# Kernel tuning notes

Hardware: AMD Instinct MI355X
Metric: run time of the kernel (lower is better)

The kernel has to match this reference:

```python
import jax, jax.numpy as jnp
import numpy as np

N_NODES = 40000
FEAT = 128
HID = 128
EMB = 64
N_EDGES = 640000


def setup_inputs() -> dict:
    key = jax.random.key(0)
    ks = jax.random.split(key, 8)
    x = jax.random.normal(ks[0], (N_NODES, FEAT), dtype=jnp.float32)
    edge_index = jax.random.randint(ks[1], (2, N_EDGES), 0, N_NODES, dtype=jnp.int64)
    s1 = 1.0 / np.sqrt(FEAT)
    s2 = 1.0 / np.sqrt(HID)
    W1_l = jax.random.uniform(ks[2], (HID, FEAT), jnp.float32, -s1, s1)
    b1 = jax.random.uniform(ks[3], (HID,), jnp.float32, -s1, s1)
    W1_r = jax.random.uniform(ks[4], (HID, FEAT), jnp.float32, -s1, s1)
    W2_l = jax.random.uniform(ks[5], (EMB, HID), jnp.float32, -s2, s2)
    b2 = jax.random.uniform(ks[6], (EMB,), jnp.float32, -s2, s2)
    W2_r = jax.random.uniform(ks[7], (EMB, HID), jnp.float32, -s2, s2)
    return {"x": x, "edge_index": edge_index, "W1_l": W1_l, "b1": b1,
            "W1_r": W1_r, "W2_l": W2_l, "b2": b2, "W2_r": W2_r}


def _sage_conv(x, src, dst, W_l, b_l, W_r, n_nodes):
    # mean aggregation of source-node features onto destination nodes
    msg = x[src]                                           # [E, d]
    agg = jax.ops.segment_sum(msg, dst, num_segments=n_nodes)   # [N, d]
    cnt = jax.ops.segment_sum(jnp.ones((src.shape[0],), x.dtype), dst,
                              num_segments=n_nodes)        # [N]
    agg = agg / jnp.maximum(cnt, 1.0)[:, None]
    # out = lin_l(mean_j x_j) + lin_r(x_i); bias lives in lin_l
    return agg @ W_l.T + b_l + x @ W_r.T


def reference(x, edge_index, W1_l, b1, W1_r, W2_l, b2, W2_r):
    src, dst = edge_index[0], edge_index[1]
    n = x.shape[0]
    h = _sage_conv(x, src, dst, W1_l, b1, W1_r, n)
    h = jax.nn.elu(h)
    # dropout p=0.2 is identity in eval mode
    h = _sage_conv(h, src, dst, W2_l, b2, W2_r, n)
    return jax.nn.log_softmax(h, axis=1)
```

## Files before the change

### kernel.cpp

```cpp
#include <hip/hip_runtime.h>
#include <hip/hip_fp16.h>
#include <math.h>

#define N_NODES 40000
#define FEATD 128
#define EMB 64
#define N_EDGES 640000
#define CAP 64
#define NB 79
#define NFB 625
#define SEGCAP 48

typedef unsigned short u16;
typedef unsigned char u8;
typedef unsigned int u32;
typedef __attribute__((ext_vector_type(8))) unsigned short u16x8;
typedef __attribute__((ext_vector_type(8))) _Float16 f16x8;
typedef __attribute__((ext_vector_type(4))) float f32x4;
typedef __attribute__((ext_vector_type(2))) float f32x2;
typedef __attribute__((ext_vector_type(2))) unsigned int u32x2;

__device__ __forceinline__ float h2f(u16 h) {
  __half hh;
  *(u16*)&hh = h;
  return __half2float(hh);
}
__device__ __forceinline__ u16 f2h(float f) {
  __half hh = __float2half(f);
  return *(u16*)&hh;
}

__global__ __launch_bounds__(256) void prep_fill_kernel(
    const float* __restrict__ x, const float* __restrict__ W1l,
    const float* __restrict__ W1r, const float* __restrict__ W2l,
    const float* __restrict__ W2r, const int* __restrict__ src,
    const int* __restrict__ dst, u16* __restrict__ xh, u8* __restrict__ xq,
    u16* __restrict__ wp, u32* __restrict__ est, u16* __restrict__ cnts) {
  __shared__ int hist[NB], starts[NB], scan[NB], cnt2[NB];
  __shared__ u32 staging[1024];
  int bid = blockIdx.x;
  int tid = threadIdx.x;
  if (bid < NFB) {
    if (tid < NB) { hist[tid] = 0; cnt2[tid] = 0; }
    __syncthreads();
    int t = bid * 256 + tid;
    int4 s4 = *(const int4*)(&src[t * 4]);
    int4 d4 = *(const int4*)(&dst[t * 4]);
    int b0 = d4.x >> 9, b1 = d4.y >> 9, b2 = d4.z >> 9, b3 = d4.w >> 9;
    atomicAdd(&hist[b0], 1); atomicAdd(&hist[b1], 1);
    atomicAdd(&hist[b2], 1); atomicAdd(&hist[b3], 1);
    __syncthreads();
    if (tid < NB) scan[tid] = hist[tid];
    for (int off = 1; off < NB; off <<= 1) {
      __syncthreads();
      int v = 0;
      if (tid < NB && tid >= off) v = scan[tid - off];
      __syncthreads();
      if (tid < NB) scan[tid] += v;
    }
    __syncthreads();
    if (tid < NB) starts[tid] = scan[tid] - hist[tid];
    __syncthreads();
    u32 e0 = ((u32)d4.x << 16) | (u32)s4.x;
    u32 e1 = ((u32)d4.y << 16) | (u32)s4.y;
    u32 e2 = ((u32)d4.z << 16) | (u32)s4.z;
    u32 e3 = ((u32)d4.w << 16) | (u32)s4.w;
    int p0 = starts[b0] + atomicAdd(&cnt2[b0], 1); staging[p0] = e0;
    int p1 = starts[b1] + atomicAdd(&cnt2[b1], 1); staging[p1] = e1;
    int p2 = starts[b2] + atomicAdd(&cnt2[b2], 1); staging[p2] = e2;
    int p3 = starts[b3] + atomicAdd(&cnt2[b3], 1); staging[p3] = e3;
    __syncthreads();
#pragma unroll
    for (int it = 0; it < 4; it++) {
      int i = tid + 256 * it;
      u32 e = staging[i];
      int b = (int)(e >> 25);
      int r = i - starts[b];
      if (r < SEGCAP) est[((size_t)b * NFB + bid) * SEGCAP + r] = e;
    }
    if (tid < NB) cnts[tid * NFB + bid] = (u16)hist[tid];
  } else if (bid < 3125) {
    int i = (bid - NFB) * 256 + tid;
    float4 v0 = *(const float4*)(&x[i * 8]);
    float4 v1 = *(const float4*)(&x[i * 8 + 4]);
    u16x8 o;
    o[0] = f2h(v0.x); o[1] = f2h(v0.y); o[2] = f2h(v0.z); o[3] = f2h(v0.w);
    o[4] = f2h(v1.x); o[5] = f2h(v1.y); o[6] = f2h(v1.z); o[7] = f2h(v1.w);
    *(u16x8*)(&xh[i * 8]) = o;
    u32 w0 = __builtin_amdgcn_cvt_pk_fp8_f32(v0.x, v0.y, 0u, false);
    w0 = __builtin_amdgcn_cvt_pk_fp8_f32(v0.z, v0.w, w0, true);
    u32 w1 = __builtin_amdgcn_cvt_pk_fp8_f32(v1.x, v1.y, 0u, false);
    w1 = __builtin_amdgcn_cvt_pk_fp8_f32(v1.z, v1.w, w1, true);
    u32x2 qo; qo.x = w0; qo.y = w1;
    *(u32x2*)(&xq[i * 8]) = qo;
  } else {
    int i = (bid - 3125) * 256 + tid;
    const float* srcp;
    int off;
    if (i < 16384)      { srcp = W1l; off = i; }
    else if (i < 32768) { srcp = W1r; off = i - 16384; }
    else if (i < 40960) { srcp = W2l; off = i - 32768; }
    else                { srcp = W2r; off = i - 40960; }
    wp[i] = f2h(srcp[off]);
  }
}

__global__ __launch_bounds__(512) void scatter_kernel(
    const u32* __restrict__ est, const u16* __restrict__ cnts,
    int* __restrict__ deg, u16* __restrict__ bucket) {
  __shared__ int ldeg[512];
  int b = blockIdx.x, tid = threadIdx.x;
  ldeg[tid] = 0;
  __syncthreads();
  int n0 = b << 9;
  for (int seg = tid; seg < NFB; seg += 512) {
    int c = cnts[b * NFB + seg];
    if (c > SEGCAP) c = SEGCAP;
    const u32* p = est + ((size_t)b * NFB + seg) * SEGCAP;
    for (int r = 0; r < c; r++) {
      u32 e = p[r];
      int l = (int)(e >> 16) - n0;
      int s = atomicAdd(&ldeg[l], 1);
      if (s < CAP) bucket[(size_t)(n0 + l) * CAP + s] = (u16)(e & 0xffff);
    }
  }
  __syncthreads();
  int n = n0 + tid;
  if (n < N_NODES) deg[n] = ldeg[tid];
}

__global__ __launch_bounds__(256) void gather_mean_f8(
    const u8* __restrict__ xq, const int* __restrict__ deg,
    const u16* __restrict__ bucket, u16* __restrict__ aggh) {
  int n = blockIdx.x * 4 + (threadIdx.x >> 6);
  int lane = threadIdx.x & 63;
  int g = lane >> 4;
  int li = lane & 15;
  int dgf = deg[n];
  int dg = dgf < CAP ? dgf : CAP;
  float inv = 1.0f / fmaxf((float)dgf, 1.0f);
  const u16* bk = bucket + n * CAP;
  float acc0[8], acc1[8], acc2[8], acc3[8];
#pragma unroll
  for (int i = 0; i < 8; i++) { acc0[i] = 0.f; acc1[i] = 0.f; acc2[i] = 0.f; acc3[i] = 0.f; }
  int d = g;
  for (; d + 12 < dg; d += 16) {
    u32x2 v0 = *(const u32x2*)(&xq[(size_t)bk[d] * 128 + li * 8]);
    u32x2 v1 = *(const u32x2*)(&xq[(size_t)bk[d + 4] * 128 + li * 8]);
    u32x2 v2 = *(const u32x2*)(&xq[(size_t)bk[d + 8] * 128 + li * 8]);
    u32x2 v3 = *(const u32x2*)(&xq[(size_t)bk[d + 12] * 128 + li * 8]);
    {
      f32x2 p0 = __builtin_amdgcn_cvt_pk_f32_fp8(v0.x, false);
      f32x2 p1 = __builtin_amdgcn_cvt_pk_f32_fp8(v0.x, true);
      f32x2 p2 = __builtin_amdgcn_cvt_pk_f32_fp8(v0.y, false);
      f32x2 p3 = __builtin_amdgcn_cvt_pk_f32_fp8(v0.y, true);
      acc0[0] += p0.x; acc0[1] += p0.y; acc0[2] += p1.x; acc0[3] += p1.y;
      acc0[4] += p2.x; acc0[5] += p2.y; acc0[6] += p3.x; acc0[7] += p3.y;
    }
    {
      f32x2 p0 = __builtin_amdgcn_cvt_pk_f32_fp8(v1.x, false);
      f32x2 p1 = __builtin_amdgcn_cvt_pk_f32_fp8(v1.x, true);
      f32x2 p2 = __builtin_amdgcn_cvt_pk_f32_fp8(v1.y, false);
      f32x2 p3 = __builtin_amdgcn_cvt_pk_f32_fp8(v1.y, true);
      acc1[0] += p0.x; acc1[1] += p0.y; acc1[2] += p1.x; acc1[3] += p1.y;
      acc1[4] += p2.x; acc1[5] += p2.y; acc1[6] += p3.x; acc1[7] += p3.y;
    }
    {
      f32x2 p0 = __builtin_amdgcn_cvt_pk_f32_fp8(v2.x, false);
      f32x2 p1 = __builtin_amdgcn_cvt_pk_f32_fp8(v2.x, true);
      f32x2 p2 = __builtin_amdgcn_cvt_pk_f32_fp8(v2.y, false);
      f32x2 p3 = __builtin_amdgcn_cvt_pk_f32_fp8(v2.y, true);
      acc2[0] += p0.x; acc2[1] += p0.y; acc2[2] += p1.x; acc2[3] += p1.y;
      acc2[4] += p2.x; acc2[5] += p2.y; acc2[6] += p3.x; acc2[7] += p3.y;
    }
    {
      f32x2 p0 = __builtin_amdgcn_cvt_pk_f32_fp8(v3.x, false);
      f32x2 p1 = __builtin_amdgcn_cvt_pk_f32_fp8(v3.x, true);
      f32x2 p2 = __builtin_amdgcn_cvt_pk_f32_fp8(v3.y, false);
      f32x2 p3 = __builtin_amdgcn_cvt_pk_f32_fp8(v3.y, true);
      acc3[0] += p0.x; acc3[1] += p0.y; acc3[2] += p1.x; acc3[3] += p1.y;
      acc3[4] += p2.x; acc3[5] += p2.y; acc3[6] += p3.x; acc3[7] += p3.y;
    }
  }
  for (; d + 4 < dg; d += 8) {
    u32x2 v0 = *(const u32x2*)(&xq[(size_t)bk[d] * 128 + li * 8]);
    u32x2 v1 = *(const u32x2*)(&xq[(size_t)bk[d + 4] * 128 + li * 8]);
    {
      f32x2 p0 = __builtin_amdgcn_cvt_pk_f32_fp8(v0.x, false);
      f32x2 p1 = __builtin_amdgcn_cvt_pk_f32_fp8(v0.x, true);
      f32x2 p2 = __builtin_amdgcn_cvt_pk_f32_fp8(v0.y, false);
      f32x2 p3 = __builtin_amdgcn_cvt_pk_f32_fp8(v0.y, true);
      acc0[0] += p0.x; acc0[1] += p0.y; acc0[2] += p1.x; acc0[3] += p1.y;
      acc0[4] += p2.x; acc0[5] += p2.y; acc0[6] += p3.x; acc0[7] += p3.y;
    }
    {
      f32x2 p0 = __builtin_amdgcn_cvt_pk_f32_fp8(v1.x, false);
      f32x2 p1 = __builtin_amdgcn_cvt_pk_f32_fp8(v1.x, true);
      f32x2 p2 = __builtin_amdgcn_cvt_pk_f32_fp8(v1.y, false);
      f32x2 p3 = __builtin_amdgcn_cvt_pk_f32_fp8(v1.y, true);
      acc1[0] += p0.x; acc1[1] += p0.y; acc1[2] += p1.x; acc1[3] += p1.y;
      acc1[4] += p2.x; acc1[5] += p2.y; acc1[6] += p3.x; acc1[7] += p3.y;
    }
  }
  if (d < dg) {
    u32x2 v0 = *(const u32x2*)(&xq[(size_t)bk[d] * 128 + li * 8]);
    f32x2 p0 = __builtin_amdgcn_cvt_pk_f32_fp8(v0.x, false);
    f32x2 p1 = __builtin_amdgcn_cvt_pk_f32_fp8(v0.x, true);
    f32x2 p2 = __builtin_amdgcn_cvt_pk_f32_fp8(v0.y, false);
    f32x2 p3 = __builtin_amdgcn_cvt_pk_f32_fp8(v0.y, true);
    acc0[0] += p0.x; acc0[1] += p0.y; acc0[2] += p1.x; acc0[3] += p1.y;
    acc0[4] += p2.x; acc0[5] += p2.y; acc0[6] += p3.x; acc0[7] += p3.y;
  }
#pragma unroll
  for (int i = 0; i < 8; i++) {
    acc0[i] += acc1[i] + acc2[i] + acc3[i];
    acc0[i] += __shfl_xor(acc0[i], 16);
    acc0[i] += __shfl_xor(acc0[i], 32);
  }
  if (g == 0) {
    u16x8 o;
#pragma unroll
    for (int i = 0; i < 8; i++) o[i] = f2h(acc0[i] * inv);
    *(u16x8*)(&aggh[n * 128 + li * 8]) = o;
  }
}

__global__ __launch_bounds__(256) void gemm12_kernel(
    const u16* __restrict__ AggH, const u16* __restrict__ XH,
    const u16* __restrict__ wp, const float* __restrict__ b1v,
    const float* __restrict__ b2v, u8* __restrict__ Yq,
    u16* __restrict__ Zh) {
  const u16* w1l = wp;
  const u16* w1r = wp + 16384;
  const u16* w2l = wp + 32768;
  const u16* w2r = wp + 40960;

  __shared__ __align__(16) union {
    struct {
      u16 wl[128][72], wr[128][72];
      u16 a[64][72], x[64][72];
    } p1;
    struct {
      u16 h[64][136];
      u16 w2l[64][136], w2r[64][136];
    } p2;
  } L;

  const int tid = threadIdx.x;
  const int wv = tid >> 6;
  const int lane = tid & 63;
  const int li = lane & 15;
  const int q = lane >> 4;
  const int nbase = blockIdx.x * 64;

  f32x4 acc1[8];
#pragma unroll
  for (int jt = 0; jt < 8; jt++) acc1[jt] = (f32x4){0.f, 0.f, 0.f, 0.f};

  for (int kb = 0; kb < 2; kb++) {
#pragma unroll
    for (int it = 0; it < 4; it++) {
      int idx = tid + 256 * it;
      int j = idx >> 3, c = idx & 7;
      int go = j * 128 + kb * 64 + c * 8;
      *(u16x8*)(&L.p1.wl[j][c * 8]) = *(const u16x8*)(&w1l[go]);
      *(u16x8*)(&L.p1.wr[j][c * 8]) = *(const u16x8*)(&w1r[go]);
    }
#pragma unroll
    for (int it = 0; it < 2; it++) {
      int idx = tid + 256 * it;
      int n = idx >> 3, c = idx & 7;
      int go = (nbase + n) * 128 + kb * 64 + c * 8;
      *(u16x8*)(&L.p1.a[n][c * 8]) = *(const u16x8*)(&AggH[go]);
      *(u16x8*)(&L.p1.x[n][c * 8]) = *(const u16x8*)(&XH[go]);
    }
    __syncthreads();
#pragma unroll
    for (int kk = 0; kk < 2; kk++) {
      f16x8 aF = *(const f16x8*)(&L.p1.a[wv * 16 + li][kk * 32 + q * 8]);
      f16x8 xF = *(const f16x8*)(&L.p1.x[wv * 16 + li][kk * 32 + q * 8]);
#pragma unroll
      for (int jt = 0; jt < 8; jt++) {
        f16x8 wlF = *(const f16x8*)(&L.p1.wl[jt * 16 + li][kk * 32 + q * 8]);
        f16x8 wrF = *(const f16x8*)(&L.p1.wr[jt * 16 + li][kk * 32 + q * 8]);
        acc1[jt] = __builtin_amdgcn_mfma_f32_16x16x32_f16(aF, wlF, acc1[jt], 0, 0, 0);
        acc1[jt] = __builtin_amdgcn_mfma_f32_16x16x32_f16(xF, wrF, acc1[jt], 0, 0, 0);
      }
    }
    __syncthreads();
  }

#pragma unroll
  for (int jt = 0; jt < 8; jt++) {
    int j = jt * 16 + li;
    float bb = b1v[j];
#pragma unroll
    for (int r = 0; r < 4; r++) {
      float v = acc1[jt][r] + bb;
      v = v > 0.f ? v : expm1f(v);
      L.p2.h[wv * 16 + q * 4 + r][j] = f2h(v);
    }
  }
#pragma unroll
  for (int it = 0; it < 4; it++) {
    int idx = tid + 256 * it;
    int j = idx >> 4, c = idx & 15;
    int go = j * 128 + c * 8;
    *(u16x8*)(&L.p2.w2l[j][c * 8]) = *(const u16x8*)(&w2l[go]);
    *(u16x8*)(&L.p2.w2r[j][c * 8]) = *(const u16x8*)(&w2r[go]);
  }
  __syncthreads();

  f32x4 accY[4], accZ[4];
#pragma unroll
  for (int mt = 0; mt < 4; mt++) {
    accY[mt] = (f32x4){0.f, 0.f, 0.f, 0.f};
    accZ[mt] = (f32x4){0.f, 0.f, 0.f, 0.f};
  }
#pragma unroll
  for (int kc = 0; kc < 4; kc++) {
    f16x8 blF = *(const f16x8*)(&L.p2.w2l[wv * 16 + li][kc * 32 + q * 8]);
    f16x8 brF = *(const f16x8*)(&L.p2.w2r[wv * 16 + li][kc * 32 + q * 8]);
#pragma unroll
    for (int mt = 0; mt < 4; mt++) {
      f16x8 hF = *(const f16x8*)(&L.p2.h[mt * 16 + li][kc * 32 + q * 8]);
      accY[mt] = __builtin_amdgcn_mfma_f32_16x16x32_f16(hF, blF, accY[mt], 0, 0, 0);
      accZ[mt] = __builtin_amdgcn_mfma_f32_16x16x32_f16(hF, brF, accZ[mt], 0, 0, 0);
    }
  }

  {
    int j2 = wv * 16 + li;
    float bb = b2v[j2];
#pragma unroll
    for (int mt = 0; mt < 4; mt++) {
#pragma unroll
      for (int r = 0; r < 4; r++) {
        int node = nbase + mt * 16 + q * 4 + r;
        float yv = accY[mt][r];
        u32 w = __builtin_amdgcn_cvt_pk_fp8_f32(yv, yv, 0u, false);
        Yq[node * 64 + j2] = (u8)w;
        Zh[node * 64 + j2] = f2h(accZ[mt][r] + bb);
      }
    }
  }
}

__global__ __launch_bounds__(256) void final_kernel(
    const u8* __restrict__ Yq, const u16* __restrict__ Zh,
    const int* __restrict__ deg, const u16* __restrict__ bucket,
    float* __restrict__ out) {
  int n = blockIdx.x * 4 + (threadIdx.x >> 6);
  int lane = threadIdx.x & 63;
  int g = lane >> 3;
  int li = lane & 7;
  int dgf = deg[n];
  int dg = dgf < CAP ? dgf : CAP;
  float inv = 1.0f / fmaxf((float)dgf, 1.0f);
  const u16* bk = bucket + n * CAP;
  float acc0[8], acc1[8];
#pragma unroll
  for (int i = 0; i < 8; i++) { acc0[i] = 0.f; acc1[i] = 0.f; }
  int d = g;
  for (; d + 8 < dg; d += 16) {
    u32x2 v0 = *(const u32x2*)(&Yq[(size_t)bk[d] * 64 + li * 8]);
    u32x2 v1 = *(const u32x2*)(&Yq[(size_t)bk[d + 8] * 64 + li * 8]);
    {
      f32x2 p0 = __builtin_amdgcn_cvt_pk_f32_fp8(v0.x, false);
      f32x2 p1 = __builtin_amdgcn_cvt_pk_f32_fp8(v0.x, true);
      f32x2 p2 = __builtin_amdgcn_cvt_pk_f32_fp8(v0.y, false);
      f32x2 p3 = __builtin_amdgcn_cvt_pk_f32_fp8(v0.y, true);
      acc0[0] += p0.x; acc0[1] += p0.y; acc0[2] += p1.x; acc0[3] += p1.y;
      acc0[4] += p2.x; acc0[5] += p2.y; acc0[6] += p3.x; acc0[7] += p3.y;
    }
    {
      f32x2 p0 = __builtin_amdgcn_cvt_pk_f32_fp8(v1.x, false);
      f32x2 p1 = __builtin_amdgcn_cvt_pk_f32_fp8(v1.x, true);
      f32x2 p2 = __builtin_amdgcn_cvt_pk_f32_fp8(v1.y, false);
      f32x2 p3 = __builtin_amdgcn_cvt_pk_f32_fp8(v1.y, true);
      acc1[0] += p0.x; acc1[1] += p0.y; acc1[2] += p1.x; acc1[3] += p1.y;
      acc1[4] += p2.x; acc1[5] += p2.y; acc1[6] += p3.x; acc1[7] += p3.y;
    }
  }
  if (d < dg) {
    u32x2 v0 = *(const u32x2*)(&Yq[(size_t)bk[d] * 64 + li * 8]);
    f32x2 p0 = __builtin_amdgcn_cvt_pk_f32_fp8(v0.x, false);
    f32x2 p1 = __builtin_amdgcn_cvt_pk_f32_fp8(v0.x, true);
    f32x2 p2 = __builtin_amdgcn_cvt_pk_f32_fp8(v0.y, false);
    f32x2 p3 = __builtin_amdgcn_cvt_pk_f32_fp8(v0.y, true);
    acc0[0] += p0.x; acc0[1] += p0.y; acc0[2] += p1.x; acc0[3] += p1.y;
    acc0[4] += p2.x; acc0[5] += p2.y; acc0[6] += p3.x; acc0[7] += p3.y;
  }
#pragma unroll
  for (int i = 0; i < 8; i++) {
    acc0[i] += acc1[i];
    acc0[i] += __shfl_xor(acc0[i], 8);
    acc0[i] += __shfl_xor(acc0[i], 16);
    acc0[i] += __shfl_xor(acc0[i], 32);
  }
  u16x8 zb = *(const u16x8*)(&Zh[n * 64 + li * 8]);
  float v[8];
#pragma unroll
  for (int i = 0; i < 8; i++) v[i] = h2f(zb[i]) + acc0[i] * inv;
  float m = v[0];
#pragma unroll
  for (int i = 1; i < 8; i++) m = fmaxf(m, v[i]);
  m = fmaxf(m, __shfl_xor(m, 1));
  m = fmaxf(m, __shfl_xor(m, 2));
  m = fmaxf(m, __shfl_xor(m, 4));
  float s = 0.f;
#pragma unroll
  for (int i = 0; i < 8; i++) s += __expf(v[i] - m);
  s += __shfl_xor(s, 1); s += __shfl_xor(s, 2); s += __shfl_xor(s, 4);
  float lg = m + logf(s);
  if (lane < 8) {
    float4 o0 = {v[0] - lg, v[1] - lg, v[2] - lg, v[3] - lg};
    float4 o1 = {v[4] - lg, v[5] - lg, v[6] - lg, v[7] - lg};
    *(float4*)(&out[n * 64 + li * 8]) = o0;
    *(float4*)(&out[n * 64 + li * 8 + 4]) = o1;
  }
}

extern "C" void kernel_launch(void* const* d_in, const int* in_sizes, int n_in,
                              void* d_out, int out_size, void* d_ws, size_t ws_size,
                              hipStream_t stream) {
  const float* x   = (const float*)d_in[0];
  const int*   ei  = (const int*)d_in[1];
  const float* W1l = (const float*)d_in[2];
  const float* b1  = (const float*)d_in[3];
  const float* W1r = (const float*)d_in[4];
  const float* W2l = (const float*)d_in[5];
  const float* b2  = (const float*)d_in[6];
  const float* W2r = (const float*)d_in[7];
  float* out = (float*)d_out;

  const int* src = ei;
  const int* dst = ei + N_EDGES;

  u16* bucket = (u16*)d_ws;
  int* deg = (int*)(bucket + (size_t)N_NODES * CAP);
  u16* xh = (u16*)(deg + N_NODES);
  u16* aggh = xh + (size_t)N_NODES * FEATD;
  u8* xq = (u8*)(aggh + (size_t)N_NODES * FEATD);
  u8* yq = xq + (size_t)N_NODES * FEATD;
  u16* zh = (u16*)(yq + (size_t)N_NODES * EMB);
  u16* wp = zh + (size_t)N_NODES * EMB;
  u32* est = (u32*)(wp + 49152);
  u16* cnts = (u16*)(est + (size_t)NB * NFB * SEGCAP);

  prep_fill_kernel<<<3317, 256, 0, stream>>>(x, W1l, W1r, W2l, W2r, src, dst,
                                             xh, xq, wp, est, cnts);
  scatter_kernel<<<NB, 512, 0, stream>>>(est, cnts, deg, bucket);
  gather_mean_f8<<<N_NODES / 4, 256, 0, stream>>>(xq, deg, bucket, aggh);
  gemm12_kernel<<<N_NODES / 64, 256, 0, stream>>>(aggh, xh, wp, b1, b2, yq, zh);
  final_kernel<<<N_NODES / 4, 256, 0, stream>>>(yq, zh, deg, bucket, out);
}
```

Baseline: 163.7 us.

## Fuse neighbor mean gather into first-layer GEMM kernel via shared memory

The separate fp8 gather/mean kernel is merged into the layer-1 GEMM kernel. Each block of 64 nodes gathers its own neighbor means directly into an LDS tile, each wave handling 16 nodes in turn, and then runs the MFMA GEMM on that tile. This removes the fp16 aggregate write and re-read through global memory and one kernel launch. In exchange the gather phase has far fewer concurrent blocks (625 vs 10000), so latency hiding for the random neighbor loads may suffer, and the enlarged LDS union may lower occupancy.

```diff
diff --git a/kernel.cpp b/kernel.cpp
--- a/kernel.cpp
+++ b/kernel.cpp
@@ -129,104 +129,9 @@
   if (n < N_NODES) deg[n] = ldeg[tid];
 }
 
-__global__ __launch_bounds__(256) void gather_mean_f8(
+__global__ __launch_bounds__(256) void gather_gemm_kernel(
     const u8* __restrict__ xq, const int* __restrict__ deg,
-    const u16* __restrict__ bucket, u16* __restrict__ aggh) {
-  int n = blockIdx.x * 4 + (threadIdx.x >> 6);
-  int lane = threadIdx.x & 63;
-  int g = lane >> 4;
-  int li = lane & 15;
-  int dgf = deg[n];
-  int dg = dgf < CAP ? dgf : CAP;
-  float inv = 1.0f / fmaxf((float)dgf, 1.0f);
-  const u16* bk = bucket + n * CAP;
-  float acc0[8], acc1[8], acc2[8], acc3[8];
-#pragma unroll
-  for (int i = 0; i < 8; i++) { acc0[i] = 0.f; acc1[i] = 0.f; acc2[i] = 0.f; acc3[i] = 0.f; }
-  int d = g;
-  for (; d + 12 < dg; d += 16) {
-    u32x2 v0 = *(const u32x2*)(&xq[(size_t)bk[d] * 128 + li * 8]);
-    u32x2 v1 = *(const u32x2*)(&xq[(size_t)bk[d + 4] * 128 + li * 8]);
-    u32x2 v2 = *(const u32x2*)(&xq[(size_t)bk[d + 8] * 128 + li * 8]);
-    u32x2 v3 = *(const u32x2*)(&xq[(size_t)bk[d + 12] * 128 + li * 8]);
-    {
-      f32x2 p0 = __builtin_amdgcn_cvt_pk_f32_fp8(v0.x, false);
-      f32x2 p1 = __builtin_amdgcn_cvt_pk_f32_fp8(v0.x, true);
-      f32x2 p2 = __builtin_amdgcn_cvt_pk_f32_fp8(v0.y, false);
-      f32x2 p3 = __builtin_amdgcn_cvt_pk_f32_fp8(v0.y, true);
-      acc0[0] += p0.x; acc0[1] += p0.y; acc0[2] += p1.x; acc0[3] += p1.y;
-      acc0[4] += p2.x; acc0[5] += p2.y; acc0[6] += p3.x; acc0[7] += p3.y;
-    }
-    {
-      f32x2 p0 = __builtin_amdgcn_cvt_pk_f32_fp8(v1.x, false);
-      f32x2 p1 = __builtin_amdgcn_cvt_pk_f32_fp8(v1.x, true);
-      f32x2 p2 = __builtin_amdgcn_cvt_pk_f32_fp8(v1.y, false);
-      f32x2 p3 = __builtin_amdgcn_cvt_pk_f32_fp8(v1.y, true);
-      acc1[0] += p0.x; acc1[1] += p0.y; acc1[2] += p1.x; acc1[3] += p1.y;
-      acc1[4] += p2.x; acc1[5] += p2.y; acc1[6] += p3.x; acc1[7] += p3.y;
-    }
-    {
-      f32x2 p0 = __builtin_amdgcn_cvt_pk_f32_fp8(v2.x, false);
-      f32x2 p1 = __builtin_amdgcn_cvt_pk_f32_fp8(v2.x, true);
-      f32x2 p2 = __builtin_amdgcn_cvt_pk_f32_fp8(v2.y, false);
-      f32x2 p3 = __builtin_amdgcn_cvt_pk_f32_fp8(v2.y, true);
-      acc2[0] += p0.x; acc2[1] += p0.y; acc2[2] += p1.x; acc2[3] += p1.y;
-      acc2[4] += p2.x; acc2[5] += p2.y; acc2[6] += p3.x; acc2[7] += p3.y;
-    }
-    {
-      f32x2 p0 = __builtin_amdgcn_cvt_pk_f32_fp8(v3.x, false);
-      f32x2 p1 = __builtin_amdgcn_cvt_pk_f32_fp8(v3.x, true);
-      f32x2 p2 = __builtin_amdgcn_cvt_pk_f32_fp8(v3.y, false);
-      f32x2 p3 = __builtin_amdgcn_cvt_pk_f32_fp8(v3.y, true);
-      acc3[0] += p0.x; acc3[1] += p0.y; acc3[2] += p1.x; acc3[3] += p1.y;
-      acc3[4] += p2.x; acc3[5] += p2.y; acc3[6] += p3.x; acc3[7] += p3.y;
-    }
-  }
-  for (; d + 4 < dg; d += 8) {
-    u32x2 v0 = *(const u32x2*)(&xq[(size_t)bk[d] * 128 + li * 8]);
-    u32x2 v1 = *(const u32x2*)(&xq[(size_t)bk[d + 4] * 128 + li * 8]);
-    {
-      f32x2 p0 = __builtin_amdgcn_cvt_pk_f32_fp8(v0.x, false);
-      f32x2 p1 = __builtin_amdgcn_cvt_pk_f32_fp8(v0.x, true);
-      f32x2 p2 = __builtin_amdgcn_cvt_pk_f32_fp8(v0.y, false);
-      f32x2 p3 = __builtin_amdgcn_cvt_pk_f32_fp8(v0.y, true);
-      acc0[0] += p0.x; acc0[1] += p0.y; acc0[2] += p1.x; acc0[3] += p1.y;
-      acc0[4] += p2.x; acc0[5] += p2.y; acc0[6] += p3.x; acc0[7] += p3.y;
-    }
-    {
-      f32x2 p0 = __builtin_amdgcn_cvt_pk_f32_fp8(v1.x, false);
-      f32x2 p1 = __builtin_amdgcn_cvt_pk_f32_fp8(v1.x, true);
-      f32x2 p2 = __builtin_amdgcn_cvt_pk_f32_fp8(v1.y, false);
-      f32x2 p3 = __builtin_amdgcn_cvt_pk_f32_fp8(v1.y, true);
-      acc1[0] += p0.x; acc1[1] += p0.y; acc1[2] += p1.x; acc1[3] += p1.y;
-      acc1[4] += p2.x; acc1[5] += p2.y; acc1[6] += p3.x; acc1[7] += p3.y;
-    }
-  }
-  if (d < dg) {
-    u32x2 v0 = *(const u32x2*)(&xq[(size_t)bk[d] * 128 + li * 8]);
-    f32x2 p0 = __builtin_amdgcn_cvt_pk_f32_fp8(v0.x, false);
-    f32x2 p1 = __builtin_amdgcn_cvt_pk_f32_fp8(v0.x, true);
-    f32x2 p2 = __builtin_amdgcn_cvt_pk_f32_fp8(v0.y, false);
-    f32x2 p3 = __builtin_amdgcn_cvt_pk_f32_fp8(v0.y, true);
-    acc0[0] += p0.x; acc0[1] += p0.y; acc0[2] += p1.x; acc0[3] += p1.y;
-    acc0[4] += p2.x; acc0[5] += p2.y; acc0[6] += p3.x; acc0[7] += p3.y;
-  }
-#pragma unroll
-  for (int i = 0; i < 8; i++) {
-    acc0[i] += acc1[i] + acc2[i] + acc3[i];
-    acc0[i] += __shfl_xor(acc0[i], 16);
-    acc0[i] += __shfl_xor(acc0[i], 32);
-  }
-  if (g == 0) {
-    u16x8 o;
-#pragma unroll
-    for (int i = 0; i < 8; i++) o[i] = f2h(acc0[i] * inv);
-    *(u16x8*)(&aggh[n * 128 + li * 8]) = o;
-  }
-}
-
-__global__ __launch_bounds__(256) void gemm12_kernel(
-    const u16* __restrict__ AggH, const u16* __restrict__ XH,
+    const u16* __restrict__ bucket, const u16* __restrict__ XH,
     const u16* __restrict__ wp, const float* __restrict__ b1v,
     const float* __restrict__ b2v, u8* __restrict__ Yq,
     u16* __restrict__ Zh) {
@@ -237,8 +142,9 @@
 
   __shared__ __align__(16) union {
     struct {
+      u16 a[64][136];
       u16 wl[128][72], wr[128][72];
-      u16 a[64][72], x[64][72];
+      u16 x[64][72];
     } p1;
     struct {
       u16 h[64][136];
@@ -251,11 +157,105 @@
   const int lane = tid & 63;
   const int li = lane & 15;
   const int q = lane >> 4;
+  const int g = lane >> 4;
   const int nbase = blockIdx.x * 64;
 
-  f32x4 acc1[8];
-#pragma unroll
-  for (int jt = 0; jt < 8; jt++) acc1[jt] = (f32x4){0.f, 0.f, 0.f, 0.f};
+  for (int i = 0; i < 16; i++) {
+    int nl = wv * 16 + i;
+    int n = nbase + nl;
+    int dgf = deg[n];
+    int dg = dgf < CAP ? dgf : CAP;
+    float inv = 1.0f / fmaxf((float)dgf, 1.0f);
+    const u16* bk = bucket + n * CAP;
+    float acc0[8], acc1[8], acc2[8], acc3[8];
+#pragma unroll
+    for (int k = 0; k < 8; k++) { acc0[k] = 0.f; acc1[k] = 0.f; acc2[k] = 0.f; acc3[k] = 0.f; }
+    int d = g;
+    for (; d + 12 < dg; d += 16) {
+      u32x2 v0 = *(const u32x2*)(&xq[(size_t)bk[d] * 128 + li * 8]);
+      u32x2 v1 = *(const u32x2*)(&xq[(size_t)bk[d + 4] * 128 + li * 8]);
+      u32x2 v2 = *(const u32x2*)(&xq[(size_t)bk[d + 8] * 128 + li * 8]);
+      u32x2 v3 = *(const u32x2*)(&xq[(size_t)bk[d + 12] * 128 + li * 8]);
+      {
+        f32x2 p0 = __builtin_amdgcn_cvt_pk_f32_fp8(v0.x, false);
+        f32x2 p1 = __builtin_amdgcn_cvt_pk_f32_fp8(v0.x, true);
+        f32x2 p2 = __builtin_amdgcn_cvt_pk_f32_fp8(v0.y, false);
+        f32x2 p3 = __builtin_amdgcn_cvt_pk_f32_fp8(v0.y, true);
+        acc0[0] += p0.x; acc0[1] += p0.y; acc0[2] += p1.x; acc0[3] += p1.y;
+        acc0[4] += p2.x; acc0[5] += p2.y; acc0[6] += p3.x; acc0[7] += p3.y;
+      }
+      {
+        f32x2 p0 = __builtin_amdgcn_cvt_pk_f32_fp8(v1.x, false);
+        f32x2 p1 = __builtin_amdgcn_cvt_pk_f32_fp8(v1.x, true);
+        f32x2 p2 = __builtin_amdgcn_cvt_pk_f32_fp8(v1.y, false);
+        f32x2 p3 = __builtin_amdgcn_cvt_pk_f32_fp8(v1.y, true);
+        acc1[0] += p0.x; acc1[1] += p0.y; acc1[2] += p1.x; acc1[3] += p1.y;
+        acc1[4] += p2.x; acc1[5] += p2.y; acc1[6] += p3.x; acc1[7] += p3.y;
+      }
+      {
+        f32x2 p0 = __builtin_amdgcn_cvt_pk_f32_fp8(v2.x, false);
+        f32x2 p1 = __builtin_amdgcn_cvt_pk_f32_fp8(v2.x, true);
+        f32x2 p2 = __builtin_amdgcn_cvt_pk_f32_fp8(v2.y, false);
+        f32x2 p3 = __builtin_amdgcn_cvt_pk_f32_fp8(v2.y, true);
+        acc2[0] += p0.x; acc2[1] += p0.y; acc2[2] += p1.x; acc2[3] += p1.y;
+        acc2[4] += p2.x; acc2[5] += p2.y; acc2[6] += p3.x; acc2[7] += p3.y;
+      }
+      {
+        f32x2 p0 = __builtin_amdgcn_cvt_pk_f32_fp8(v3.x, false);
+        f32x2 p1 = __builtin_amdgcn_cvt_pk_f32_fp8(v3.x, true);
+        f32x2 p2 = __builtin_amdgcn_cvt_pk_f32_fp8(v3.y, false);
+        f32x2 p3 = __builtin_amdgcn_cvt_pk_f32_fp8(v3.y, true);
+        acc3[0] += p0.x; acc3[1] += p0.y; acc3[2] += p1.x; acc3[3] += p1.y;
+        acc3[4] += p2.x; acc3[5] += p2.y; acc3[6] += p3.x; acc3[7] += p3.y;
+      }
+    }
+    for (; d + 4 < dg; d += 8) {
+      u32x2 v0 = *(const u32x2*)(&xq[(size_t)bk[d] * 128 + li * 8]);
+      u32x2 v1 = *(const u32x2*)(&xq[(size_t)bk[d + 4] * 128 + li * 8]);
+      {
+        f32x2 p0 = __builtin_amdgcn_cvt_pk_f32_fp8(v0.x, false);
+        f32x2 p1 = __builtin_amdgcn_cvt_pk_f32_fp8(v0.x, true);
+        f32x2 p2 = __builtin_amdgcn_cvt_pk_f32_fp8(v0.y, false);
+        f32x2 p3 = __builtin_amdgcn_cvt_pk_f32_fp8(v0.y, true);
+        acc0[0] += p0.x; acc0[1] += p0.y; acc0[2] += p1.x; acc0[3] += p1.y;
+        acc0[4] += p2.x; acc0[5] += p2.y; acc0[6] += p3.x; acc0[7] += p3.y;
+      }
+      {
+        f32x2 p0 = __builtin_amdgcn_cvt_pk_f32_fp8(v1.x, false);
+        f32x2 p1 = __builtin_amdgcn_cvt_pk_f32_fp8(v1.x, true);
+        f32x2 p2 = __builtin_amdgcn_cvt_pk_f32_fp8(v1.y, false);
+        f32x2 p3 = __builtin_amdgcn_cvt_pk_f32_fp8(v1.y, true);
+        acc1[0] += p0.x; acc1[1] += p0.y; acc1[2] += p1.x; acc1[3] += p1.y;
+        acc1[4] += p2.x; acc1[5] += p2.y; acc1[6] += p3.x; acc1[7] += p3.y;
+      }
+    }
+    if (d < dg) {
+      u32x2 v0 = *(const u32x2*)(&xq[(size_t)bk[d] * 128 + li * 8]);
+      f32x2 p0 = __builtin_amdgcn_cvt_pk_f32_fp8(v0.x, false);
+      f32x2 p1 = __builtin_amdgcn_cvt_pk_f32_fp8(v0.x, true);
+      f32x2 p2 = __builtin_amdgcn_cvt_pk_f32_fp8(v0.y, false);
+      f32x2 p3 = __builtin_amdgcn_cvt_pk_f32_fp8(v0.y, true);
+      acc0[0] += p0.x; acc0[1] += p0.y; acc0[2] += p1.x; acc0[3] += p1.y;
+      acc0[4] += p2.x; acc0[5] += p2.y; acc0[6] += p3.x; acc0[7] += p3.y;
+    }
+#pragma unroll
+    for (int k = 0; k < 8; k++) {
+      acc0[k] += acc1[k] + acc2[k] + acc3[k];
+      acc0[k] += __shfl_xor(acc0[k], 16);
+      acc0[k] += __shfl_xor(acc0[k], 32);
+    }
+    if (g == 0) {
+      u16x8 o;
+#pragma unroll
+      for (int k = 0; k < 8; k++) o[k] = f2h(acc0[k] * inv);
+      *(u16x8*)(&L.p1.a[nl][li * 8]) = o;
+    }
+  }
+  __syncthreads();
+
+  f32x4 acc1g[8];
+#pragma unroll
+  for (int jt = 0; jt < 8; jt++) acc1g[jt] = (f32x4){0.f, 0.f, 0.f, 0.f};
 
   for (int kb = 0; kb < 2; kb++) {
 #pragma unroll
@@ -271,20 +271,19 @@
       int idx = tid + 256 * it;
       int n = idx >> 3, c = idx & 7;
       int go = (nbase + n) * 128 + kb * 64 + c * 8;
-      *(u16x8*)(&L.p1.a[n][c * 8]) = *(const u16x8*)(&AggH[go]);
       *(u16x8*)(&L.p1.x[n][c * 8]) = *(const u16x8*)(&XH[go]);
     }
     __syncthreads();
 #pragma unroll
     for (int kk = 0; kk < 2; kk++) {
-      f16x8 aF = *(const f16x8*)(&L.p1.a[wv * 16 + li][kk * 32 + q * 8]);
+      f16x8 aF = *(const f16x8*)(&L.p1.a[wv * 16 + li][kb * 64 + kk * 32 + q * 8]);
       f16x8 xF = *(const f16x8*)(&L.p1.x[wv * 16 + li][kk * 32 + q * 8]);
 #pragma unroll
       for (int jt = 0; jt < 8; jt++) {
         f16x8 wlF = *(const f16x8*)(&L.p1.wl[jt * 16 + li][kk * 32 + q * 8]);
         f16x8 wrF = *(const f16x8*)(&L.p1.wr[jt * 16 + li][kk * 32 + q * 8]);
-        acc1[jt] = __builtin_amdgcn_mfma_f32_16x16x32_f16(aF, wlF, acc1[jt], 0, 0, 0);
-        acc1[jt] = __builtin_amdgcn_mfma_f32_16x16x32_f16(xF, wrF, acc1[jt], 0, 0, 0);
+        acc1g[jt] = __builtin_amdgcn_mfma_f32_16x16x32_f16(aF, wlF, acc1g[jt], 0, 0, 0);
+        acc1g[jt] = __builtin_amdgcn_mfma_f32_16x16x32_f16(xF, wrF, acc1g[jt], 0, 0, 0);
       }
     }
     __syncthreads();
@@ -296,7 +295,7 @@
     float bb = b1v[j];
 #pragma unroll
     for (int r = 0; r < 4; r++) {
-      float v = acc1[jt][r] + bb;
+      float v = acc1g[jt][r] + bb;
       v = v > 0.f ? v : expm1f(v);
       L.p2.h[wv * 16 + q * 4 + r][j] = f2h(v);
     }
@@ -440,8 +439,7 @@
   u16* bucket = (u16*)d_ws;
   int* deg = (int*)(bucket + (size_t)N_NODES * CAP);
   u16* xh = (u16*)(deg + N_NODES);
-  u16* aggh = xh + (size_t)N_NODES * FEATD;
-  u8* xq = (u8*)(aggh + (size_t)N_NODES * FEATD);
+  u8* xq = (u8*)(xh + (size_t)N_NODES * FEATD);
   u8* yq = xq + (size_t)N_NODES * FEATD;
   u16* zh = (u16*)(yq + (size_t)N_NODES * EMB);
   u16* wp = zh + (size_t)N_NODES * EMB;
@@ -451,7 +449,7 @@
   prep_fill_kernel<<<3317, 256, 0, stream>>>(x, W1l, W1r, W2l, W2r, src, dst,
                                              xh, xq, wp, est, cnts);
   scatter_kernel<<<NB, 512, 0, stream>>>(est, cnts, deg, bucket);
-  gather_mean_f8<<<N_NODES / 4, 256, 0, stream>>>(xq, deg, bucket, aggh);
-  gemm12_kernel<<<N_NODES / 64, 256, 0, stream>>>(aggh, xh, wp, b1, b2, yq, zh);
+  gather_gemm_kernel<<<N_NODES / 64, 256, 0, stream>>>(xq, deg, bucket, xh, wp,
+                                                       b1, b2, yq, zh);
   final_kernel<<<N_NODES / 4, 256, 0, stream>>>(yq, zh, deg, bucket, out);
 }
```

After: 204.2 us. 24.7% more time.
